# Kernel tuning notes

Hardware: AMD Instinct MI355X
Metric: run time of the kernel (lower is better)

The kernel has to match this reference:

```python
import jax, jax.numpy as jnp
import numpy as np

THR1 = 0.8     # lif1 threshold
THR2 = 1.0     # lif2 (Synaptic) default threshold
ALPHA2 = 0.9   # Synaptic alpha (not learnable, use_stdp=False)
BETA2 = 0.8    # Synaptic beta
SLOPE = 25.0   # snntorch fast_sigmoid default slope

@jax.custom_vjp
def fast_sigmoid_spike(x):
    return (x > 0).astype(x.dtype)

def _fs_fwd(x):
    return fast_sigmoid_spike(x), x

def _fs_bwd(x, g):
    return (g / (SLOPE * jnp.abs(x) + 1.0) ** 2,)

fast_sigmoid_spike.defvjp(_fs_fwd, _fs_bwd)

@jax.custom_vjp
def atan_spike(x):  # snntorch default ATan surrogate, alpha=2.0
    return (x > 0).astype(x.dtype)

def _at_fwd(x):
    return atan_spike(x), x

def _at_bwd(x, g):
    return (g / (1.0 + (jnp.pi * x) ** 2),)

atan_spike.defvjp(_at_fwd, _at_bwd)

def setup_inputs() -> dict:
    key = jax.random.key(0)
    k = jax.random.split(key, 6)
    B, S, V, H, E, T = 16, 16, 16000, 512, 256, 20
    x = jax.random.randint(k[0], (B, S), 0, V)
    embed_w = jax.random.normal(k[1], (V, E), dtype=jnp.float32)  # torch Embedding ~ N(0,1)
    fc1_w = jax.random.normal(k[2], (H, E), dtype=jnp.float32) / np.sqrt(E)
    fc1_b = jax.random.normal(k[3], (H,), dtype=jnp.float32) / np.sqrt(E)
    fc2_w = jax.random.normal(k[4], (V, H), dtype=jnp.float32) / np.sqrt(H)
    fc2_b = jax.random.normal(k[5], (V,), dtype=jnp.float32) / np.sqrt(H)
    beta1 = jnp.float32(0.85)  # learnable Leaky beta
    return {"x": x, "embed_w": embed_w, "fc1_w": fc1_w, "fc1_b": fc1_b,
            "fc2_w": fc2_w, "fc2_b": fc2_b, "beta1": beta1, "time_steps": T}

def reference(x, embed_w, fc1_w, fc1_b, fc2_w, fc2_b, beta1, time_steps):
    B, S = x.shape
    H = fc1_w.shape[0]
    V = fc2_w.shape[0]
    emb = embed_w[x]                       # [B, S, 256]
    b1 = jnp.clip(beta1, 0.0, 1.0)
    mem1 = jnp.zeros((B, H), emb.dtype)
    syn2 = jnp.zeros((B, V), emb.dtype)
    mem2 = jnp.zeros((B, V), emb.dtype)

    def token_step(carry, emb_t):          # emb_t: [B, 256]
        mem1, syn2, mem2 = carry
        cur1 = emb_t @ fc1_w.T + fc1_b     # identical every inner step (hoisted)

        def inner(c, _):
            m1, s2, m2, _ = c
            reset = fast_sigmoid_spike(m1 - THR1)          # reset from previous mem
            m1 = b1 * m1 + cur1 - reset * THR1             # Leaky, subtract reset
            spk1 = fast_sigmoid_spike(m1 - THR1)
            cur2 = spk1 @ fc2_w.T + fc2_b                  # [B, V]
            s2 = ALPHA2 * s2 + cur2                        # Synaptic, reset='none'
            m2 = BETA2 * m2 + s2
            spk2 = atan_spike(m2 - THR2)
            return (m1, s2, m2, spk2), None

        (mem1, syn2, mem2, spk2), _ = jax.lax.scan(
            inner, (mem1, syn2, mem2, jnp.zeros_like(mem2)), None, length=time_steps)
        return (mem1, syn2, mem2), spk2    # keep last spk2 of inner loop

    (mem1, syn2, mem2), outs = jax.lax.scan(
        token_step, (mem1, syn2, mem2), jnp.swapaxes(emb, 0, 1))  # scan over seq
    out = jnp.transpose(outs, (1, 0, 2))   # [B, S, V]
    return out, mem1, syn2, mem2
```

## Files before the change

### kernel.cpp

```cpp
#include <hip/hip_runtime.h>

#define Bdim 16
#define Sdim 16
#define Edim 256
#define Hdim 512
#define Vdim 16000
#define THR1f 0.8f
#define THR2f 1.0f

typedef unsigned int   u32;
typedef unsigned short u16;
typedef __attribute__((ext_vector_type(8))) short bf16x8;
typedef __attribute__((ext_vector_type(4))) float f32x4;

__device__ __forceinline__ u16 f2bf(float f) {
  u32 u = __float_as_uint(f);
  return (u16)((u + 0x7FFFu + ((u >> 16) & 1u)) >> 16);
}
__device__ __forceinline__ float bf2f(u16 u) {
  return __uint_as_float(((u32)u) << 16);
}
__device__ __forceinline__ void gload16(const void* g, const void* lds) {
  __builtin_amdgcn_global_load_lds(
      (const __attribute__((address_space(1))) u32*)g,
      (__attribute__((address_space(3))) u32*)lds, 16, 0, 0);
}

__global__ __launch_bounds__(256) void w2bf(const float* __restrict__ W,
                                            u16* __restrict__ Wb) {
  const size_t id = (size_t)blockIdx.x * 256 + threadIdx.x;
  const float4* s = (const float4*)W;
  const float4 a = s[id * 2], b = s[id * 2 + 1];
  uint4 o;
  o.x = (u32)f2bf(a.x) | ((u32)f2bf(a.y) << 16);
  o.y = (u32)f2bf(a.z) | ((u32)f2bf(a.w) << 16);
  o.z = (u32)f2bf(b.x) | ((u32)f2bf(b.y) << 16);
  o.w = (u32)f2bf(b.z) | ((u32)f2bf(b.w) << 16);
  ((uint4*)Wb)[id] = o;
}

__global__ __launch_bounds__(256) void snn_cur1(
    const int* __restrict__ x, const float* __restrict__ embed_w,
    const float* __restrict__ fc1_w, const float* __restrict__ fc1_b,
    float* __restrict__ cur1)
{
  __shared__ __align__(16) float As[64][68];
  __shared__ __align__(16) float Ws[64][68];
  __shared__ int sidx[64];
  const int tid = threadIdx.x;
  const int n0 = blockIdx.x * 64, r0 = blockIdx.y * 64;
  const int tx = tid & 15, ty = tid >> 4;

  if (tid < 64) {
    const int r1 = r0 + tid;
    sidx[tid] = x[(r1 & 15) * Sdim + (r1 >> 4)];
  }

  float acc[4][4] = {{0.f}};
  for (int k0 = 0; k0 < Edim; k0 += 64) {
    __syncthreads();
#pragma unroll
    for (int i = 0; i < 16; ++i) {
      const int k = tid + i * 256;
      const int rr = k >> 6, j = k & 63;
      As[j][rr] = embed_w[(size_t)sidx[rr] * Edim + k0 + j];
      Ws[j][rr] = fc1_w[(size_t)(n0 + rr) * Edim + k0 + j];
    }
    __syncthreads();
#pragma unroll
    for (int j = 0; j < 64; ++j) {
      const float4 av = *(const float4*)&As[j][ty * 4];
      const float4 wv = *(const float4*)&Ws[j][tx * 4];
      const float a[4] = {av.x, av.y, av.z, av.w};
      const float w[4] = {wv.x, wv.y, wv.z, wv.w};
#pragma unroll
      for (int i = 0; i < 4; ++i)
#pragma unroll
        for (int jj = 0; jj < 4; ++jj)
          acc[i][jj] = fmaf(a[i], w[jj], acc[i][jj]);
    }
  }
#pragma unroll
  for (int i = 0; i < 4; ++i) {
    float4 o;
    o.x = acc[i][0] + fc1_b[n0 + tx * 4 + 0];
    o.y = acc[i][1] + fc1_b[n0 + tx * 4 + 1];
    o.z = acc[i][2] + fc1_b[n0 + tx * 4 + 2];
    o.w = acc[i][3] + fc1_b[n0 + tx * 4 + 3];
    *(float4*)&cur1[(size_t)(r0 + ty * 4 + i) * Hdim + n0 + tx * 4] = o;
  }
}

__global__ __launch_bounds__(256) void snn_rec(
    const float* __restrict__ cur1, const float* __restrict__ beta1p,
    const int* __restrict__ tsp, u16* __restrict__ Ab,
    float* __restrict__ mem1)
{
  const int id = blockIdx.x * 256 + threadIdx.x;
  const int b = id >> 9, h = id & 511;
  const float b1 = fminf(fmaxf(beta1p[0], 0.f), 1.f);
  const int T = tsp[0];

  double w9T = 1.0, w8T = 1.0;
  for (int i = 0; i < T; ++i) { w9T *= 0.9; w8T *= 0.8; }

  float m1 = 0.f;
  for (int t = 0; t < Sdim; ++t) {
    const float cur = cur1[(size_t)(t * Bdim + b) * Hdim + h];
    double p9 = w9T, p8 = w8T;
    float cs = 0.f, cm = 0.f;
    for (int u = 0; u < T; ++u) {
      const float reset = (m1 > THR1f) ? THR1f : 0.f;
      m1 = b1 * m1 + cur - reset;
      if (m1 > THR1f) {
        cs += (float)(p9 * (10.0 / 9.0));
        cm += (float)(10.0 * (p9 - p8));
      }
      p9 *= (10.0 / 9.0);
      p8 *= 1.25;
    }
    const size_t r = (size_t)(t * Bdim + b) * 2;
    Ab[r * Hdim + h]       = f2bf(cs);
    Ab[(r + 1) * Hdim + h] = f2bf(cm);
  }
  mem1[b * Hdim + h] = m1;
}

__global__ __launch_bounds__(256) void snn_mfma(
    const u16* __restrict__ Ab, const u16* __restrict__ Wb,
    u16* __restrict__ Cb)
{
  __shared__ __align__(16) u16 As[128 * 64];
  __shared__ __align__(16) u16 Bs[128 * 64];
  const int tid  = threadIdx.x;
  const int lane = tid & 63;
  const int wid  = tid >> 6;
  const int wm   = wid >> 1, wn = wid & 1;
  const int v0 = blockIdx.x * 128;
  const int r0 = blockIdx.y * 128;

  f32x4 acc[4][4];
#pragma unroll
  for (int i = 0; i < 4; ++i)
#pragma unroll
    for (int j = 0; j < 4; ++j)
#pragma unroll
      for (int e = 0; e < 4; ++e) acc[i][j][e] = 0.f;

  char* AsB = (char*)As;
  char* BsB = (char*)Bs;

  for (int k0 = 0; k0 < Hdim; k0 += 64) {
#pragma unroll
    for (int rnd = 0; rnd < 4; ++rnd) {
      const int base = (rnd * 4 + wid) << 10;
      const int flat = base + lane * 16;
      const int row  = flat >> 7;
      const int cl   = (flat & 127) ^ ((row & 7) << 4);
      gload16(Ab + (((size_t)(r0 + row)) << 9) + k0 + (cl >> 1), AsB + base);
      gload16(Wb + (((size_t)(v0 + row)) << 9) + k0 + (cl >> 1), BsB + base);
    }
    __syncthreads();
#pragma unroll
    for (int kk = 0; kk < 2; ++kk) {
      const int cbase = kk * 64 + ((lane >> 4) << 4);
      bf16x8 af[4], bfr[4];
#pragma unroll
      for (int i = 0; i < 4; ++i) {
        const int ar = wm * 64 + i * 16 + (lane & 15);
        af[i]  = *(const bf16x8*)(AsB + ar * 128 + (cbase ^ ((ar & 7) << 4)));
        const int br = wn * 64 + i * 16 + (lane & 15);
        bfr[i] = *(const bf16x8*)(BsB + br * 128 + (cbase ^ ((br & 7) << 4)));
      }
#pragma unroll
      for (int mi = 0; mi < 4; ++mi)
#pragma unroll
        for (int ni = 0; ni < 4; ++ni)
          acc[mi][ni] = __builtin_amdgcn_mfma_f32_16x16x32_bf16(
              af[mi], bfr[ni], acc[mi][ni], 0, 0, 0);
    }
    __syncthreads();
  }

  const int cn = lane & 15, rq = (lane >> 4) * 4;
#pragma unroll
  for (int mi = 0; mi < 4; ++mi) {
    const int rrow = r0 + wm * 64 + mi * 16 + rq;
#pragma unroll
    for (int ni = 0; ni < 4; ++ni) {
      const int ccol = v0 + wn * 64 + ni * 16 + cn;
#pragma unroll
      for (int e = 0; e < 4; ++e)
        Cb[(size_t)(rrow + e) * Vdim + ccol] = f2bf(acc[mi][ni][e]);
    }
  }
}

__global__ __launch_bounds__(256) void snn_epi(
    const u16* __restrict__ Cb, const float* __restrict__ fc2_b,
    const int* __restrict__ tsp,
    float* __restrict__ out, float* __restrict__ syn2, float* __restrict__ mem2)
{
  const int id = blockIdx.x * 256 + threadIdx.x;
  if (id >= Bdim * Vdim) return;
  const int v = id % Vdim;
  const int b = id / Vdim;
  const int T = tsp[0];

  double p9 = 1.0, p8 = 1.0;
  for (int i = 0; i < T; ++i) { p9 *= 0.9; p8 *= 0.8; }
  const float Ps  = (float)p9;
  const float Pm  = (float)p8;
  const float Pms = (float)(0.9 * 10.0 * (p9 - p8));
  const float Sws = (float)(10.0 * (1.0 - p9));
  const float Swm = (float)(10.0 * (9.0 * (1.0 - p9) - 4.0 * (1.0 - p8)));

  const float bb  = fc2_b[v];
  const float bbs = bb * Sws;
  const float bbm = bb * Swm;

  float s2 = 0.f, m2 = 0.f;
#pragma unroll
  for (int t = 0; t < Sdim; ++t) {
    const size_t r = (size_t)(t * Bdim + b) * 2;
    const float gs = bf2f(Cb[r * Vdim + v]);
    const float gm = bf2f(Cb[(r + 1) * Vdim + v]);
    const float m2n = Pm * m2 + Pms * s2 + gm + bbm;
    s2 = Ps * s2 + gs + bbs;
    m2 = m2n;
    out[((size_t)b * Sdim + t) * Vdim + v] = (m2 > THR2f) ? 1.f : 0.f;
  }
  syn2[(size_t)b * Vdim + v] = s2;
  mem2[(size_t)b * Vdim + v] = m2;
}

extern "C" void kernel_launch(void* const* d_in, const int* in_sizes, int n_in,
                              void* d_out, int out_size, void* d_ws, size_t ws_size,
                              hipStream_t stream) {
  const int*   x       = (const int*)d_in[0];
  const float* embed_w = (const float*)d_in[1];
  const float* fc1_w   = (const float*)d_in[2];
  const float* fc1_b   = (const float*)d_in[3];
  const float* fc2_w   = (const float*)d_in[4];
  const float* fc2_b   = (const float*)d_in[5];
  const float* beta1   = (const float*)d_in[6];
  const int*   tsteps  = (const int*)d_in[7];

  float* out  = (float*)d_out;
  float* mem1 = out + (size_t)Bdim * Sdim * Vdim;
  float* syn2 = mem1 + (size_t)Bdim * Hdim;
  float* mem2 = syn2 + (size_t)Bdim * Vdim;

  float* cur1 = (float*)d_ws;
  u16*   Ab   = (u16*)((char*)d_ws + 524288);
  u16*   Wb   = (u16*)((char*)d_ws + 1048576);
  u16*   Cb   = (u16*)((char*)d_ws + 1048576 + 16384000);

  w2bf<<<4000, 256, 0, stream>>>(fc2_w, Wb);
  snn_cur1<<<dim3(Hdim / 64, (Sdim * Bdim) / 64), 256, 0, stream>>>(
      x, embed_w, fc1_w, fc1_b, cur1);
  snn_rec<<<(Bdim * Hdim) / 256, 256, 0, stream>>>(cur1, beta1, tsteps, Ab, mem1);
  snn_mfma<<<dim3(Vdim / 128, (2 * Sdim * Bdim) / 128), 256, 0, stream>>>(Ab, Wb, Cb);
  snn_epi<<<(Bdim * Vdim + 255) / 256, 256, 0, stream>>>(Cb, fc2_b, tsteps,
                                                         out, syn2, mem2);
}
```

Baseline: 158.5 us.

## Fuse weight conversion, fc2 GEMM and synaptic epilogue into one kernel

Measured after the change: 156.3 us. About the same (-1.4%).

```diff
diff --git a/kernel.cpp b/kernel.cpp
--- a/kernel.cpp
+++ b/kernel.cpp
@@ -17,26 +17,13 @@
   u32 u = __float_as_uint(f);
   return (u16)((u + 0x7FFFu + ((u >> 16) & 1u)) >> 16);
 }
-__device__ __forceinline__ float bf2f(u16 u) {
-  return __uint_as_float(((u32)u) << 16);
+__device__ __forceinline__ u32 pack2(float a, float b) {
+  return (u32)f2bf(a) | ((u32)f2bf(b) << 16);
 }
 __device__ __forceinline__ void gload16(const void* g, const void* lds) {
   __builtin_amdgcn_global_load_lds(
       (const __attribute__((address_space(1))) u32*)g,
       (__attribute__((address_space(3))) u32*)lds, 16, 0, 0);
-}
-
-__global__ __launch_bounds__(256) void w2bf(const float* __restrict__ W,
-                                            u16* __restrict__ Wb) {
-  const size_t id = (size_t)blockIdx.x * 256 + threadIdx.x;
-  const float4* s = (const float4*)W;
-  const float4 a = s[id * 2], b = s[id * 2 + 1];
-  uint4 o;
-  o.x = (u32)f2bf(a.x) | ((u32)f2bf(a.y) << 16);
-  o.y = (u32)f2bf(a.z) | ((u32)f2bf(a.w) << 16);
-  o.z = (u32)f2bf(b.x) | ((u32)f2bf(b.y) << 16);
-  o.w = (u32)f2bf(b.z) | ((u32)f2bf(b.w) << 16);
-  ((uint4*)Wb)[id] = o;
 }
 
 __global__ __launch_bounds__(256) void snn_cur1(
@@ -126,87 +113,73 @@
   mem1[b * Hdim + h] = m1;
 }
 
-__global__ __launch_bounds__(256) void snn_mfma(
-    const u16* __restrict__ Ab, const u16* __restrict__ Wb,
-    u16* __restrict__ Cb)
+__global__ __launch_bounds__(256) void snn_fused(
+    const u16* __restrict__ Ab, const float* __restrict__ W,
+    const float* __restrict__ fc2_b, const int* __restrict__ tsp,
+    float* __restrict__ out, float* __restrict__ syn2, float* __restrict__ mem2)
 {
-  __shared__ __align__(16) u16 As[128 * 64];
-  __shared__ __align__(16) u16 Bs[128 * 64];
+  __shared__ __align__(16) u16 As[512 * 64];
+  __shared__ __align__(16) u16 Bs[64 * 64];
   const int tid  = threadIdx.x;
   const int lane = tid & 63;
   const int wid  = tid >> 6;
-  const int wm   = wid >> 1, wn = wid & 1;
-  const int v0 = blockIdx.x * 128;
-  const int r0 = blockIdx.y * 128;
-
-  f32x4 acc[4][4];
-#pragma unroll
-  for (int i = 0; i < 4; ++i)
-#pragma unroll
-    for (int j = 0; j < 4; ++j)
-#pragma unroll
-      for (int e = 0; e < 4; ++e) acc[i][j][e] = 0.f;
+  const int v0   = blockIdx.x * 64;
+
+  f32x4 acc[32];
+#pragma unroll
+  for (int i = 0; i < 32; ++i)
+#pragma unroll
+    for (int e = 0; e < 4; ++e) acc[i][e] = 0.f;
 
   char* AsB = (char*)As;
   char* BsB = (char*)Bs;
 
+  const int brow = tid >> 2;
+  const int bkc  = (tid & 3) * 16;
+  const int bswz = (brow & 7) << 4;
+
   for (int k0 = 0; k0 < Hdim; k0 += 64) {
 #pragma unroll
-    for (int rnd = 0; rnd < 4; ++rnd) {
-      const int base = (rnd * 4 + wid) << 10;
+    for (int rnd = 0; rnd < 16; ++rnd) {
+      const int base = rnd * 4096 + wid * 1024;
       const int flat = base + lane * 16;
       const int row  = flat >> 7;
       const int cl   = (flat & 127) ^ ((row & 7) << 4);
-      gload16(Ab + (((size_t)(r0 + row)) << 9) + k0 + (cl >> 1), AsB + base);
-      gload16(Wb + (((size_t)(v0 + row)) << 9) + k0 + (cl >> 1), BsB + base);
+      gload16(Ab + ((size_t)row << 9) + k0 + (cl >> 1), AsB + base);
+    }
+    {
+      const float4* wp =
+          (const float4*)&W[(size_t)(v0 + brow) * Hdim + k0 + bkc];
+      const float4 w0 = wp[0], w1 = wp[1], w2 = wp[2], w3 = wp[3];
+      uint4 o0, o1;
+      o0.x = pack2(w0.x, w0.y); o0.y = pack2(w0.z, w0.w);
+      o0.z = pack2(w1.x, w1.y); o0.w = pack2(w1.z, w1.w);
+      o1.x = pack2(w2.x, w2.y); o1.y = pack2(w2.z, w2.w);
+      o1.z = pack2(w3.x, w3.y); o1.w = pack2(w3.z, w3.w);
+      const int cb = bkc * 2;
+      *(uint4*)(BsB + brow * 128 + (cb ^ bswz)) = o0;
+      *(uint4*)(BsB + brow * 128 + ((cb + 16) ^ bswz)) = o1;
     }
     __syncthreads();
 #pragma unroll
     for (int kk = 0; kk < 2; ++kk) {
       const int cbase = kk * 64 + ((lane >> 4) << 4);
-      bf16x8 af[4], bfr[4];
-#pragma unroll
-      for (int i = 0; i < 4; ++i) {
-        const int ar = wm * 64 + i * 16 + (lane & 15);
-        af[i]  = *(const bf16x8*)(AsB + ar * 128 + (cbase ^ ((ar & 7) << 4)));
-        const int br = wn * 64 + i * 16 + (lane & 15);
-        bfr[i] = *(const bf16x8*)(BsB + br * 128 + (cbase ^ ((br & 7) << 4)));
+      const int br = wid * 16 + (lane & 15);
+      const bf16x8 bfr =
+          *(const bf16x8*)(BsB + br * 128 + (cbase ^ ((br & 7) << 4)));
+#pragma unroll
+      for (int mi = 0; mi < 32; ++mi) {
+        const int ar = mi * 16 + (lane & 15);
+        const bf16x8 af =
+            *(const bf16x8*)(AsB + ar * 128 + (cbase ^ ((ar & 7) << 4)));
+        acc[mi] = __builtin_amdgcn_mfma_f32_16x16x32_bf16(af, bfr, acc[mi],
+                                                          0, 0, 0);
       }
-#pragma unroll
-      for (int mi = 0; mi < 4; ++mi)
-#pragma unroll
-        for (int ni = 0; ni < 4; ++ni)
-          acc[mi][ni] = __builtin_amdgcn_mfma_f32_16x16x32_bf16(
-              af[mi], bfr[ni], acc[mi][ni], 0, 0, 0);
-    }
-    __syncthreads();
-  }
-
-  const int cn = lane & 15, rq = (lane >> 4) * 4;
-#pragma unroll
-  for (int mi = 0; mi < 4; ++mi) {
-    const int rrow = r0 + wm * 64 + mi * 16 + rq;
-#pragma unroll
-    for (int ni = 0; ni < 4; ++ni) {
-      const int ccol = v0 + wn * 64 + ni * 16 + cn;
-#pragma unroll
-      for (int e = 0; e < 4; ++e)
-        Cb[(size_t)(rrow + e) * Vdim + ccol] = f2bf(acc[mi][ni][e]);
-    }
-  }
-}
-
-__global__ __launch_bounds__(256) void snn_epi(
-    const u16* __restrict__ Cb, const float* __restrict__ fc2_b,
-    const int* __restrict__ tsp,
-    float* __restrict__ out, float* __restrict__ syn2, float* __restrict__ mem2)
-{
-  const int id = blockIdx.x * 256 + threadIdx.x;
-  if (id >= Bdim * Vdim) return;
-  const int v = id % Vdim;
-  const int b = id / Vdim;
+    }
+    __syncthreads();
+  }
+
   const int T = tsp[0];
-
   double p9 = 1.0, p8 = 1.0;
   for (int i = 0; i < T; ++i) { p9 *= 0.9; p8 *= 0.8; }
   const float Ps  = (float)p9;
@@ -215,23 +188,31 @@
   const float Sws = (float)(10.0 * (1.0 - p9));
   const float Swm = (float)(10.0 * (9.0 * (1.0 - p9) - 4.0 * (1.0 - p8)));
 
+  const int g = lane >> 4;
+  const int v = v0 + wid * 16 + (lane & 15);
   const float bb  = fc2_b[v];
   const float bbs = bb * Sws;
   const float bbm = bb * Swm;
 
-  float s2 = 0.f, m2 = 0.f;
-#pragma unroll
-  for (int t = 0; t < Sdim; ++t) {
-    const size_t r = (size_t)(t * Bdim + b) * 2;
-    const float gs = bf2f(Cb[r * Vdim + v]);
-    const float gm = bf2f(Cb[(r + 1) * Vdim + v]);
-    const float m2n = Pm * m2 + Pms * s2 + gm + bbm;
-    s2 = Ps * s2 + gs + bbs;
-    m2 = m2n;
-    out[((size_t)b * Sdim + t) * Vdim + v] = (m2 > THR2f) ? 1.f : 0.f;
-  }
-  syn2[(size_t)b * Vdim + v] = s2;
-  mem2[(size_t)b * Vdim + v] = m2;
+#pragma unroll
+  for (int hi = 0; hi < 2; ++hi) {
+#pragma unroll
+    for (int j = 0; j < 2; ++j) {
+      const int b = hi * 8 + 2 * g + j;
+      float s2 = 0.f, m2 = 0.f;
+#pragma unroll
+      for (int t = 0; t < Sdim; ++t) {
+        const float gs = acc[2 * t + hi][2 * j];
+        const float gm = acc[2 * t + hi][2 * j + 1];
+        const float m2n = Pm * m2 + Pms * s2 + gm + bbm;
+        s2 = Ps * s2 + gs + bbs;
+        m2 = m2n;
+        out[((size_t)b * Sdim + t) * Vdim + v] = (m2 > THR2f) ? 1.f : 0.f;
+      }
+      syn2[(size_t)b * Vdim + v] = s2;
+      mem2[(size_t)b * Vdim + v] = m2;
+    }
+  }
 }
 
 extern "C" void kernel_launch(void* const* d_in, const int* in_sizes, int n_in,
@@ -253,14 +234,10 @@
 
   float* cur1 = (float*)d_ws;
   u16*   Ab   = (u16*)((char*)d_ws + 524288);
-  u16*   Wb   = (u16*)((char*)d_ws + 1048576);
-  u16*   Cb   = (u16*)((char*)d_ws + 1048576 + 16384000);
-
-  w2bf<<<4000, 256, 0, stream>>>(fc2_w, Wb);
+
   snn_cur1<<<dim3(Hdim / 64, (Sdim * Bdim) / 64), 256, 0, stream>>>(
       x, embed_w, fc1_w, fc1_b, cur1);
   snn_rec<<<(Bdim * Hdim) / 256, 256, 0, stream>>>(cur1, beta1, tsteps, Ab, mem1);
-  snn_mfma<<<dim3(Vdim / 128, (2 * Sdim * Bdim) / 128), 256, 0, stream>>>(Ab, Wb, Cb);
-  snn_epi<<<(Bdim * Vdim + 255) / 256, 256, 0, stream>>>(Cb, fc2_b, tsteps,
-                                                         out, syn2, mem2);
-}
+  snn_fused<<<Vdim / 64, 256, 0, stream>>>(Ab, fc2_w, fc2_b, tsteps,
+                                           out, syn2, mem2);
+}
```
